# Kernel optimization log

Hardware: AMD Instinct MI355X
Metric: run time of the kernel (lower is better)

## Reference

```python
import jax, jax.numpy as jnp
import numpy as np

Q_DIM, T_DIM, TOP_M, TEMP = 512, 768, 5, 0.07
B, H, W, K = 8, 64, 64, 128
LN_EPS = 1e-5

def _layernorm(x, g, b):
    mu = jnp.mean(x, axis=-1, keepdims=True)
    var = jnp.mean(jnp.square(x - mu), axis=-1, keepdims=True)
    return (x - mu) * jax.lax.rsqrt(var + LN_EPS) * g + b

def _l2norm(x):
    n = jnp.linalg.norm(x, axis=-1, keepdims=True)
    return x / jnp.maximum(n, 1e-12)

def setup_inputs() -> dict:
    key = jax.random.key(0)
    ks = jax.random.split(key, 12)
    s = lambda d: 1.0 / np.sqrt(d)
    return {
        'visual_features': jax.random.normal(ks[0], (B, H, W, Q_DIM), jnp.float32),
        'text_features': jax.random.normal(ks[1], (B, K, T_DIM), jnp.float32),
        'Wq': jax.random.uniform(ks[2], (Q_DIM, T_DIM), jnp.float32, -s(Q_DIM), s(Q_DIM)),
        'bq': jnp.zeros((T_DIM,), jnp.float32),
        'Wv': jax.random.uniform(ks[3], (T_DIM, Q_DIM), jnp.float32, -s(T_DIM), s(T_DIM)),
        'bv': jnp.zeros((Q_DIM,), jnp.float32),
        'W1': jax.random.uniform(ks[4], (Q_DIM, 4 * Q_DIM), jnp.float32, -s(Q_DIM), s(Q_DIM)),
        'b1': jnp.zeros((4 * Q_DIM,), jnp.float32),
        'W2': jax.random.uniform(ks[5], (4 * Q_DIM, Q_DIM), jnp.float32, -s(4 * Q_DIM), s(4 * Q_DIM)),
        'b2': jnp.zeros((Q_DIM,), jnp.float32),
        'g1': jnp.ones((Q_DIM,), jnp.float32), 'be1': jnp.zeros((Q_DIM,), jnp.float32),
        'g2': jnp.ones((Q_DIM,), jnp.float32), 'be2': jnp.zeros((Q_DIM,), jnp.float32),
    }

def reference(visual_features, text_features, Wq, bq, Wv, bv, W1, b1, W2, b2, g1, be1, g2, be2):
    b, h, w, c = visual_features.shape
    residual = visual_features.reshape(b, h * w, c)
    vis = _layernorm(residual, g1, be1)                      # (B,N,C)
    query = _l2norm(vis @ Wq + bq)                            # (B,N,Ct)
    keyt = _l2norm(text_features)                             # (B,K,Ct)
    value = text_features @ Wv + bv                           # (B,K,C)
    sim = jnp.einsum('bnc,bkc->bnk', query, keyt)             # (B,N,K)
    # top-M sparsification: keep top_m logits, others -> -inf
    top_v = jax.lax.top_k(sim, TOP_M)[0]                      # (B,N,M) sorted desc
    thr = top_v[..., -1:]
    sim = jnp.where(sim >= thr, sim, -jnp.inf)
    attn = jax.nn.softmax(sim / TEMP, axis=-1)
    aligned = jnp.einsum('bnk,bkc->bnc', attn, value)
    fused = residual + aligned
    fused = _layernorm(fused, g2, be2)
    ffn = jax.nn.gelu(fused @ W1 + b1, approximate=False) @ W2 + b2
    out = fused + ffn
    return out.reshape(b, h, w, c)
```

## Files before the change

### kernel.cpp

```cpp
#include <hip/hip_runtime.h>
#include <math.h>

typedef unsigned short u16;
typedef unsigned int   u32;
typedef unsigned long long u64;
typedef __attribute__((ext_vector_type(4))) float f32x4;
typedef __attribute__((ext_vector_type(4))) unsigned int u32x4;
typedef __attribute__((ext_vector_type(8))) _Float16 f16x8;
typedef __attribute__((ext_vector_type(8))) short s16x8;

#define NROWS   32768
#define CDIM    512
#define TDIM    768
#define KKEY    128
#define FFDIM   2048
#define NB      8
#define RPB     4096
#define LN_EPS_ 1e-5f
#define TINV    (1.0f/0.07f)
#define RESCUE_MARGIN 1e-5f

__device__ __forceinline__ u16 f2h(float f){ _Float16 h=(_Float16)f; return __builtin_bit_cast(u16,h); }
__device__ __forceinline__ float h2f(u16 v){ return (float)__builtin_bit_cast(_Float16, v); }
__device__ __forceinline__ unsigned pk2(float a,float b){ return (unsigned)f2h(a)|((unsigned)f2h(b)<<16); }
__device__ __forceinline__ u16 f2b(float f){
  u32 u = __builtin_bit_cast(u32, f);
  u32 r = (u + 0x7fffu + ((u>>16)&1u)) >> 16;
  return (u16)r;
}
__device__ __forceinline__ float b2f(u16 h){ u32 u = ((u32)h)<<16; return __builtin_bit_cast(float, u); }
__device__ __forceinline__ unsigned pkb(float a,float b){ return (unsigned)f2b(a)|((unsigned)f2b(b)<<16); }

__device__ __forceinline__ void gl_lds16(const void* g, void* l){
  __builtin_amdgcn_global_load_lds(
      (const __attribute__((address_space(1))) u32*)g,
      (__attribute__((address_space(3))) u32*)l, 16, 0, 0);
}

__device__ __forceinline__ float fast_exp2(float x){
#if __has_builtin(__builtin_amdgcn_exp2f)
  return __builtin_amdgcn_exp2f(x);
#else
  return exp2f(x);
#endif
}
__device__ __forceinline__ float fast_rcp(float x){
#if __has_builtin(__builtin_amdgcn_rcpf)
  return __builtin_amdgcn_rcpf(x);
#else
  return 1.0f/x;
#endif
}

__device__ __forceinline__ float wsumf(float v){
#pragma unroll
  for(int o=1;o<64;o<<=1) v+=__shfl_xor(v,o);
  return v; }
__device__ __forceinline__ float wmaxf(float v){
#pragma unroll
  for(int o=1;o<64;o<<=1) v=fmaxf(v,__shfl_xor(v,o));
  return v; }
__device__ __forceinline__ double wsumd(double v){
#pragma unroll
  for(int o=1;o<64;o<<=1) v+=__shfl_xor(v,o);
  return v; }
__device__ __forceinline__ double wmaxd(double v){
#pragma unroll
  for(int o=1;o<64;o<<=1){ double t=__shfl_xor(v,o); v = t>v ? t : v; }
  return v; }

__device__ __forceinline__ double blocksumd4(double v, double* red){
  const int lane = threadIdx.x & 63, w = threadIdx.x >> 6;
  v = wsumd(v);
  __syncthreads();
  if (lane==0) red[w] = v;
  __syncthreads();
  return red[0]+red[1]+red[2]+red[3];
}

template<int R, int C, int MODE>
__device__ __forceinline__ void tr_tile(const float* __restrict__ in, void* __restrict__ out,
                                        int bx, int by, float (*tile)[33])
{
  int c0 = bx*32, r0 = by*32;
  int tx = threadIdx.x, ty = threadIdx.y;
#pragma unroll
  for (int i=0;i<4;i++){
    int r = r0 + ty + i*8;
    tile[ty+i*8][tx] = in[(size_t)r*C + c0 + tx];
  }
  __syncthreads();
#pragma unroll
  for (int i=0;i<4;i++){
    int cc = c0 + ty + i*8, rr = r0 + tx;
    float v = tile[tx][ty+i*8];
    if (MODE==1)      ((u16*)out)[(size_t)cc*R + rr] = f2h(v);
    else if (MODE==2) ((u16*)out)[(size_t)cc*R + rr] = f2b(v);
    else              ((float*)out)[(size_t)cc*R + rr] = v;
  }
}

__global__ __launch_bounds__(256) void transpose_all_kernel(
    const float* __restrict__ Wq, const float* __restrict__ W1,
    const float* __restrict__ W2, const float* __restrict__ Wv,
    u16* __restrict__ Wqbt, u16* __restrict__ W116t,
    u16* __restrict__ W216t, float* __restrict__ WvT)
{
  __shared__ float tile[32][33];
  int bid = blockIdx.x;
  if (bid < 384){
    tr_tile<512,768,2>(Wq, Wqbt, bid%24, bid/24, tile);
  } else if (bid < 1408){
    int b = bid-384;  tr_tile<512,2048,1>(W1, W116t, b%64, b/64, tile);
  } else if (bid < 2432){
    int b = bid-1408; tr_tile<2048,512,1>(W2, W216t, b%16, b/16, tile);
  } else {
    int b = bid-2432; tr_tile<768,512,0>(Wv, WvT, b%16, b/16, tile);
  }
}

__global__ __launch_bounds__(256) void keystats_kernel(
    const float* __restrict__ text, const float* __restrict__ bq,
    float* __restrict__ normk, float* __restrict__ crr)
{
  int gw = blockIdx.x*4 + (threadIdx.x>>6);
  int lane = threadIdx.x & 63;
  const float* tr = &text[(size_t)gw*TDIM];
  double ss=0.0, db=0.0;
#pragma unroll
  for (int i=0;i<12;i++){
    float v = tr[lane + 64*i];
    ss += (double)v*(double)v;
    db += (double)bq[lane+64*i]*(double)v;
  }
  ss = wsumd(ss); db = wsumd(db);
  if (lane==0){
    double nk = sqrt(ss); nk = nk>1e-12 ? nk : 1e-12;
    normk[gw] = (float)nk;
    crr[gw]   = (float)db;
  }
}

__global__ __launch_bounds__(256) void ln1_kernel(
    const float* __restrict__ visual, const float* __restrict__ g1, const float* __restrict__ be1,
    u16* __restrict__ visH, u16* __restrict__ visL)
{
  int row = blockIdx.x*4 + (threadIdx.x>>6);
  int lane = threadIdx.x & 63;
  size_t base = (size_t)row*CDIM + lane*8;
  f32x4 a = *(const f32x4*)&visual[base];
  f32x4 c = *(const f32x4*)&visual[base+4];
  float s = a[0]+a[1]+a[2]+a[3]+c[0]+c[1]+c[2]+c[3];
  s = wsumf(s);
  float mu = s * (1.0f/512.0f);
  float q = 0.f;
#pragma unroll
  for (int i=0;i<4;i++){ float d=a[i]-mu; q+=d*d; }
#pragma unroll
  for (int i=0;i<4;i++){ float d=c[i]-mu; q+=d*d; }
  q = wsumf(q);
  float rs = rsqrtf(q*(1.0f/512.0f) + LN_EPS_);
  int cb = lane*8;
  float o[8];
#pragma unroll
  for (int i=0;i<4;i++) o[i]   = (a[i]-mu)*rs*g1[cb+i]   + be1[cb+i];
#pragma unroll
  for (int i=0;i<4;i++) o[4+i] = (c[i]-mu)*rs*g1[cb+4+i] + be1[cb+4+i];
  u16 hh[8];
  float lo[8];
#pragma unroll
  for (int i=0;i<8;i++){ hh[i] = f2b(o[i]); lo[i] = o[i] - b2f(hh[i]); }
  u32x4 hv, lv;
#pragma unroll
  for (int i=0;i<4;i++){
    hv[i] = (u32)hh[2*i] | ((u32)hh[2*i+1]<<16);
    lv[i] = pkb(lo[2*i], lo[2*i+1]);
  }
  *(u32x4*)&visH[base] = hv;
  *(u32x4*)&visL[base] = lv;
}

__global__ __launch_bounds__(256) void gemm_txt_kernel(
    const float* __restrict__ text, const float* __restrict__ Wq,
    const float* __restrict__ WvT,
    u16* __restrict__ MrtH, u16* __restrict__ MrtL, float* __restrict__ value)
{
  __shared__ float As[64][17];
  __shared__ float Bs[64][17];
  const int zz = blockIdx.z;
  const bool isV = zz >= 8;
  const int z = isV ? zz-8 : zz;
  const float* A  = text + (size_t)z*KKEY*TDIM;
  const float* Bt = isV ? WvT : Wq;
  const int tid = threadIdx.x;
  const int tx = tid & 15, ty = tid >> 4;
  const int m0 = blockIdx.x*64, n0 = blockIdx.y*64;
  float acc[4][4];
#pragma unroll
  for (int i=0;i<4;i++)
#pragma unroll
    for (int j=0;j<4;j++) acc[i][j]=0.f;
  const int lr = tid >> 2, lc = (tid & 3)*4;
  for (int k0=0; k0<TDIM; k0+=16){
    f32x4 av = *(const f32x4*)&A [(size_t)(m0+lr)*TDIM + k0 + lc];
    f32x4 bv = *(const f32x4*)&Bt[(size_t)(n0+lr)*TDIM + k0 + lc];
#pragma unroll
    for (int i=0;i<4;i++){ As[lr][lc+i]=av[i]; Bs[lr][lc+i]=bv[i]; }
    __syncthreads();
#pragma unroll
    for (int kk=0; kk<16; kk++){
      float a[4], b[4];
#pragma unroll
      for (int i=0;i<4;i++){ a[i]=As[ty*4+i][kk]; b[i]=Bs[tx*4+i][kk]; }
#pragma unroll
      for (int i=0;i<4;i++)
#pragma unroll
        for (int j=0;j<4;j++) acc[i][j] = fmaf(a[i], b[j], acc[i][j]);
    }
    __syncthreads();
  }
#pragma unroll
  for (int i=0;i<4;i++){
    size_t idx = ((size_t)z*KKEY + m0 + ty*4 + i)*CDIM + n0 + tx*4;
    if (isV){
      f32x4 o;
#pragma unroll
      for (int j=0;j<4;j++) o[j]=acc[i][j];
      *(f32x4*)&value[idx] = o;
    } else {
      u16 hh[4]; u16 ll[4];
#pragma unroll
      for (int j=0;j<4;j++){
        float v = acc[i][j];
        u16 h = f2b(v);
        hh[j] = h;
        ll[j] = f2b(v - b2f(h));
      }
      ((u32*)&MrtH[idx])[0] = (u32)hh[0] | ((u32)hh[1]<<16);
      ((u32*)&MrtH[idx])[1] = (u32)hh[2] | ((u32)hh[3]<<16);
      ((u32*)&MrtL[idx])[0] = (u32)ll[0] | ((u32)ll[1]<<16);
      ((u32*)&MrtL[idx])[1] = (u32)ll[2] | ((u32)ll[3]<<16);
    }
  }
}

__device__ __forceinline__ float gelu_exact(float v){
  float x  = v*0.70710678118654752440f;
  float ax = fabsf(x);
  float t  = fast_rcp(fmaf(0.3275911f, ax, 1.0f));
  float p  = t*fmaf(t, fmaf(t, fmaf(t, fmaf(t, 1.061405429f, -1.453152027f),
                  1.421413741f), -0.284496736f), 0.254829592f);
  float e  = fast_exp2(ax*ax*(-1.4426950408889634f));
  float y  = 1.0f - p*e;
  float er = (x < 0.0f) ? -y : y;
  return 0.5f*v*(1.0f + er);
}

template<int EPI, int NN, int KK, int NT>
__global__ __launch_bounds__(256) void gemm_f16_kernel(
    const u16* __restrict__ A, const u16* __restrict__ Bt,
    const float* __restrict__ bias,
    float* __restrict__ out_f,
    u16* __restrict__ out_h,
    const u16* __restrict__ add_h)
{
  __shared__ __align__(16) u16 As[2][128*64];
  __shared__ __align__(16) u16 Bs[2][128*64];
  const int tid = threadIdx.x;
  const int lane = tid & 63, w = tid >> 6;
  const int wr = w >> 1, wc = w & 1;
  constexpr int NWG = 256*NT;
  const int wg = blockIdx.x;
  const int b2 = (wg & 7)*(NWG/8) + (wg >> 3);
  const int ntile = b2 % NT, mtile = b2 / NT;
  const int m0 = mtile*128, n0 = ntile*128;
  f32x4 acc[4][4];
#pragma unroll
  for (int i=0;i<4;i++)
#pragma unroll
    for (int j=0;j<4;j++) acc[i][j] = (f32x4)0.f;
  const int lr = lane & 15, lk = (lane >> 4)*8;
  const int c8_sw = ((lane & 7) ^ (lane >> 3))*8;
  const size_t stride32 = (size_t)32*KK;
  const u16* aBase = &A [(size_t)(m0 + w*8 + (lane>>3))*KK + c8_sw];
  const u16* bBase = &Bt[(size_t)(n0 + w*8 + (lane>>3))*KK + c8_sw];

  auto STAGE = [&](int buf, int k0){
#pragma unroll
    for (int i=0;i<4;i++){
      gl_lds16(aBase + i*stride32 + k0, &As[buf][w*512 + i*2048]);
      gl_lds16(bBase + i*stride32 + k0, &Bs[buf][w*512 + i*2048]);
    }
  };

  STAGE(0, 0);
  int cur = 0;
  for (int k0=0; k0<KK; k0+=64){
    if (k0 + 64 < KK){
      STAGE(cur^1, k0+64);
      asm volatile("s_waitcnt vmcnt(8)" ::: "memory");
    } else {
      asm volatile("s_waitcnt vmcnt(0)" ::: "memory");
    }
    __builtin_amdgcn_s_barrier();
#pragma unroll
    for (int kk=0; kk<64; kk+=32){
      s16x8 af[4], bfv[4];
      const int csw = (kk + lk) ^ ((lr & 7) << 3);
#pragma unroll
      for (int mi=0;mi<4;mi++) af[mi]  = *(const s16x8*)&As[cur][(wr*64 + mi*16 + lr)*64 + csw];
#pragma unroll
      for (int ni=0;ni<4;ni++) bfv[ni] = *(const s16x8*)&Bs[cur][(wc*64 + ni*16 + lr)*64 + csw];
#pragma unroll
      for (int mi=0;mi<4;mi++)
#pragma unroll
        for (int ni=0;ni<4;ni++){
          if (EPI == 0)
            acc[mi][ni] = __builtin_amdgcn_mfma_f32_16x16x32_bf16(af[mi], bfv[ni], acc[mi][ni], 0, 0, 0);
          else
            acc[mi][ni] = __builtin_amdgcn_mfma_f32_16x16x32_f16(
                __builtin_bit_cast(f16x8, af[mi]), __builtin_bit_cast(f16x8, bfv[ni]), acc[mi][ni], 0, 0, 0);
        }
    }
    __builtin_amdgcn_s_barrier();
    cur ^= 1;
  }
  const int lr4 = (lane >> 4)*4;
  if (EPI == 0){
    float sq[4][4];
#pragma unroll
    for (int mi=0;mi<4;mi++)
#pragma unroll
      for (int r=0;r<4;r++) sq[mi][r]=0.f;
#pragma unroll
    for (int ni=0;ni<4;ni++){
      float bqv = bias[n0 + wc*64 + ni*16 + lr];
#pragma unroll
      for (int mi=0;mi<4;mi++)
#pragma unroll
        for (int r=0;r<4;r++){
          float v = acc[mi][ni][r] + bqv;
          sq[mi][r] += v*v;
        }
    }
#pragma unroll
    for (int o=1;o<16;o<<=1)
#pragma unroll
      for (int mi=0;mi<4;mi++)
#pragma unroll
        for (int r=0;r<4;r++) sq[mi][r] += __shfl_xor(sq[mi][r], o);
    if ((lane & 15) == 0){
      int part = ntile*2 + wc;
#pragma unroll
      for (int mi=0;mi<4;mi++)
#pragma unroll
        for (int r=0;r<4;r++){
          int row = m0 + wr*64 + mi*16 + lr4 + r;
          out_f[(size_t)row*12 + part] = sq[mi][r];
        }
    }
  } else {
    const int row0 = m0 + wr*64 + lr4;
    const int col0 = n0 + wc*64 + lr;
    float bb[4];
#pragma unroll
    for (int ni=0;ni<4;ni++) bb[ni] = bias[col0 + ni*16];
    if (EPI == 1){
      u16* op = out_h + (size_t)row0*NN + col0;
#pragma unroll
      for (int mi=0;mi<4;mi++)
#pragma unroll
        for (int r=0;r<4;r++)
#pragma unroll
          for (int ni=0;ni<4;ni++)
            op[(size_t)(mi*16+r)*NN + ni*16] = f2h(gelu_exact(acc[mi][ni][r] + bb[ni]));
    } else {
      float* op = out_f + (size_t)row0*NN + col0;
      const u16* rp = add_h + (size_t)row0*NN + col0;
#pragma unroll
      for (int mi=0;mi<4;mi++)
#pragma unroll
        for (int r=0;r<4;r++)
#pragma unroll
          for (int ni=0;ni<4;ni++)
            op[(size_t)(mi*16+r)*NN + ni*16] =
                acc[mi][ni][r] + bb[ni] + h2f(rp[(size_t)(mi*16+r)*NN + ni*16]);
    }
  }
}

__global__ __launch_bounds__(256) void gemm_t_kernel(
    const u16* __restrict__ Ah, const u16* __restrict__ Al,
    const u16* __restrict__ Bh, const u16* __restrict__ Bl,
    float* __restrict__ C)
{
  __shared__ __align__(16) u16 As[2][128*64];
  __shared__ __align__(16) u16 Bs[2][128*64];
  const int tid = threadIdx.x;
  const int lane = tid & 63, w = tid >> 6;
  const int wr = w >> 1, wc = w & 1;
  const int mtile = blockIdx.x;
  const int p = blockIdx.y;
  const int m0 = mtile*128, z = mtile >> 5;
  const u16* Ap = (p==2) ? Al : Ah;
  const u16* Bp = (p==1) ? Bl : Bh;
  f32x4 acc[4][4];
#pragma unroll
  for (int i=0;i<4;i++)
#pragma unroll
    for (int j=0;j<4;j++) acc[i][j] = (f32x4)0.f;
  const int lr = lane & 15, lk = (lane >> 4)*8;
  const int c8_sw = ((lane & 7) ^ (lane >> 3))*8;
  const size_t aOff = (size_t)(m0 + w*8 + (lane>>3))*CDIM + c8_sw;
  const size_t bOff = (size_t)(z*KKEY + w*8 + (lane>>3))*CDIM + c8_sw;
  const size_t stride32 = (size_t)32*CDIM;

  auto STAGE = [&](int buf, int s){
    const int k0 = s << 6;
#pragma unroll
    for (int i=0;i<4;i++){
      gl_lds16(Ap + aOff + i*stride32 + k0, &As[buf][w*512 + i*2048]);
      gl_lds16(Bp + bOff + i*stride32 + k0, &Bs[buf][w*512 + i*2048]);
    }
  };

  STAGE(0, 0);
  int cur = 0;
  for (int s=0; s<8; ++s){
    if (s < 7){
      STAGE(cur^1, s+1);
      asm volatile("s_waitcnt vmcnt(8)" ::: "memory");
    } else {
      asm volatile("s_waitcnt vmcnt(0)" ::: "memory");
    }
    __builtin_amdgcn_s_barrier();
#pragma unroll
    for (int kk=0; kk<64; kk+=32){
      s16x8 af[4], bfv[4];
      const int csw = (kk + lk) ^ ((lr & 7) << 3);
#pragma unroll
      for (int mi=0;mi<4;mi++) af[mi]  = *(const s16x8*)&As[cur][(wr*64 + mi*16 + lr)*64 + csw];
#pragma unroll
      for (int ni=0;ni<4;ni++) bfv[ni] = *(const s16x8*)&Bs[cur][(wc*64 + ni*16 + lr)*64 + csw];
#pragma unroll
      for (int mi=0;mi<4;mi++)
#pragma unroll
        for (int ni=0;ni<4;ni++)
          acc[mi][ni] = __builtin_amdgcn_mfma_f32_16x16x32_bf16(af[mi], bfv[ni], acc[mi][ni], 0, 0, 0);
    }
    __builtin_amdgcn_s_barrier();
    cur ^= 1;
  }
  const int lr4 = (lane >> 4)*4;
  const int row0 = m0 + wr*64 + lr4;
  const int col0 = wc*64 + lr;
  float* op = C + (size_t)p*NROWS*KKEY + (size_t)row0*KKEY + col0;
#pragma unroll
  for (int mi=0;mi<4;mi++)
#pragma unroll
    for (int r=0;r<4;r++)
#pragma unroll
      for (int ni=0;ni<4;ni++)
        op[(size_t)(mi*16+r)*KKEY + ni*16] = acc[mi][ni][r];
}

__global__ __launch_bounds__(256) void rescue_kernel(
    const int* __restrict__ rcnt, const int* __restrict__ rlist,
    const float* __restrict__ visual, const float* __restrict__ text,
    const float* __restrict__ Wq, const float* __restrict__ bq,
    const float* __restrict__ g1, const float* __restrict__ be1,
    const float* __restrict__ g2, const float* __restrict__ be2,
    const float* __restrict__ value, const float* __restrict__ bv,
    u16* __restrict__ fused16)
{
  __shared__ double vis64[512];
  __shared__ double q64[768];
  __shared__ double sims[128];
  __shared__ double pw[128];
  __shared__ double red[4];
  __shared__ double sc2[2];
  __shared__ int klist[128];
  __shared__ int kcount;
  const int tid = threadIdx.x, lane = tid & 63, w = tid >> 6;
  int n = *rcnt; if (n > NROWS) n = NROWS;
  for (int i = blockIdx.x; i < n; i += gridDim.x){
    const int row = rlist[i], b = row >> 12;
    const size_t rb = (size_t)row*CDIM;
    double x0 = (double)visual[rb+tid], x1 = (double)visual[rb+tid+256];
    double s = blocksumd4(x0+x1, red);
    double mu = s*(1.0/512.0);
    double d0 = x0-mu, d1 = x1-mu;
    double var = blocksumd4(d0*d0+d1*d1, red);
    double rs = 1.0/sqrt(var*(1.0/512.0) + 1e-5);
    vis64[tid]     = d0*rs*(double)g1[tid]     + (double)be1[tid];
    vis64[tid+256] = d1*rs*(double)g1[tid+256] + (double)be1[tid+256];
    __syncthreads();
    double qa0=(double)bq[tid], qa1=(double)bq[tid+256], qa2=(double)bq[tid+512];
#pragma unroll 4
    for (int c=0;c<CDIM;c++){
      double v = vis64[c];
      const float* wrow = &Wq[(size_t)c*TDIM];
      qa0 += v*(double)wrow[tid];
      qa1 += v*(double)wrow[tid+256];
      qa2 += v*(double)wrow[tid+512];
    }
    q64[tid]=qa0; q64[tid+256]=qa1; q64[tid+512]=qa2;
    double nq2 = blocksumd4(qa0*qa0+qa1*qa1+qa2*qa2, red);
    double nq = sqrt(nq2); if (nq < 1e-12) nq = 1e-12;
    __syncthreads();
    if (tid < KKEY){
      const float* trow = &text[((size_t)b*KKEY + tid)*TDIM];
      double dot=0.0, nk2=0.0;
#pragma unroll 8
      for (int j=0;j<TDIM;j++){
        double tv = (double)trow[j];
        dot += q64[j]*tv; nk2 += tv*tv;
      }
      double nk = sqrt(nk2); if (nk < 1e-12) nk = 1e-12;
      sims[tid] = dot/(nq*nk);
    }
    __syncthreads();
    if (w == 0){
      double v0=sims[lane], v1=sims[lane+64];
      bool rm0=false, rm1=false;
      double thr=0.0, smax=0.0;
      for (int it=0; it<5; ++it){
        double c0 = rm0 ? -1e300 : v0;
        double c1 = rm1 ? -1e300 : v1;
        double m = wmaxd(c0>c1 ? c0 : c1);
        if (it==0) smax = m;
        thr = m;
        bool h0 = (!rm0) && (v0==m);
        u64 k0 = __ballot(h0);
        if (k0){ if (lane == __ffsll(k0)-1) rm0 = true; }
        else {
          bool h1 = (!rm1) && (v1==m);
          u64 k1 = __ballot(h1);
          if (lane == __ffsll(k1)-1) rm1 = true;
        }
      }
      if (lane==0){ sc2[0]=smax; sc2[1]=thr; kcount=0; }
    }
    __syncthreads();
    const double smax = sc2[0], thr = sc2[1];
    double p = 0.0;
    if (tid < KKEY){
      double sv = sims[tid];
      p = (sv >= thr) ? exp((sv-smax)*(1.0/0.07)) : 0.0;
      pw[tid] = p;
      if (p > 0.0){ int pos = atomicAdd(&kcount, 1); klist[pos] = tid; }
    }
    double Z = blocksumd4(p, red);
    double zi = 1.0/Z;
    __syncthreads();
    double a0=(double)bv[tid], a1=(double)bv[tid+256];
    int kc = kcount;
    for (int ki=0; ki<kc; ++ki){
      int k = klist[ki];
      double wt = pw[k]*zi;
      const float* vr = &value[((size_t)b*KKEY + k)*CDIM];
      a0 += wt*(double)vr[tid];
      a1 += wt*(double)vr[tid+256];
    }
    double f0 = (double)visual[rb+tid]     + a0;
    double f1 = (double)visual[rb+tid+256] + a1;
    double fsum = blocksumd4(f0+f1, red);
    double fmu = fsum*(1.0/512.0);
    double e0=f0-fmu, e1=f1-fmu;
    double fvar = blocksumd4(e0*e0+e1*e1, red);
    double frs = 1.0/sqrt(fvar*(1.0/512.0) + 1e-5);
    fused16[rb+tid]     = f2h((float)(e0*frs*(double)g2[tid]     + (double)be2[tid]));
    fused16[rb+tid+256] = f2h((float)(e1*frs*(double)g2[tid+256] + (double)be2[tid+256]));
    __syncthreads();
  }
}

__global__ __launch_bounds__(256) void attn_ln2_kernel(
    const float* __restrict__ visual,
    const float* __restrict__ tbuf, const float* __restrict__ crr,
    const float* __restrict__ normk, const float* __restrict__ qpart,
    const float* __restrict__ value, const float* __restrict__ bv,
    const float* __restrict__ g2, const float* __restrict__ be2,
    u16* __restrict__ fused16,
    int* __restrict__ rcnt, int* __restrict__ rlist)
{
  const int w = threadIdx.x >> 6, lane = threadIdx.x & 63;
  const int row = blockIdx.x*4 + w;
  const int b = row >> 12;
  float nqp = (lane < 12) ? qpart[(size_t)row*12 + lane] : 0.f;
  float nq2 = wsumf(nqp);
  float nq = fmaxf(sqrtf(nq2), 1e-12f);
  const float* t0 = &tbuf[(size_t)row*KKEY];
  const float* t1 = t0 + (size_t)NROWS*KKEY;
  const float* t2 = t1 + (size_t)NROWS*KKEY;
  float ta = t0[lane]    + t1[lane]    + t2[lane];
  float tb = t0[lane+64] + t1[lane+64] + t2[lane+64];
  float s0 = (ta + crr[b*KKEY + lane])    / (nq*normk[b*KKEY + lane]);
  float s1 = (tb + crr[b*KKEY + lane+64]) / (nq*normk[b*KKEY + lane+64]);
  float v0=s0, v1=s1; bool rm0=false, rm1=false;
  float thr=0.f, smax=0.f, m6=0.f;
  for (int it=0; it<6; ++it){
    float c0 = rm0 ? -1e30f : v0;
    float c1 = rm1 ? -1e30f : v1;
    float m = wmaxf(fmaxf(c0,c1));
    if (it==0) smax = m;
    if (it<5){
      thr = m;
      bool h0 = (!rm0) && (v0==m);
      u64 k0 = __ballot(h0);
      if (k0){ if (lane == __ffsll(k0)-1) rm0 = true; }
      else {
        bool h1 = (!rm1) && (v1==m);
        u64 k1 = __ballot(h1);
        if (lane == __ffsll(k1)-1) rm1 = true;
      }
    } else m6 = m;
  }
  if ((thr - m6) < RESCUE_MARGIN){
    if (lane == 0){
      int p = atomicAdd(rcnt, 1);
      rlist[p] = row;
    }
    return;
  }
  float p0 = (s0>=thr) ? expf((s0-smax)*TINV) : 0.f;
  float p1 = (s1>=thr) ? expf((s1-smax)*TINV) : 0.f;
  float Z = wsumf(p0+p1);
  float zi = 1.f/Z;
  float accv[8];
#pragma unroll
  for (int j=0;j<8;j++) accv[j] = bv[lane*8+j];
  u64 mk0 = __ballot(p0>0.f);
  u64 mk1 = __ballot(p1>0.f);
  while (mk0){
    int l = __ffsll(mk0)-1; mk0 &= mk0-1;
    float wt = __shfl(p0, l)*zi;
    const f32x4* vr = (const f32x4*)&value[((size_t)b*KKEY + l)*CDIM + lane*8];
    f32x4 va = vr[0], vb = vr[1];
#pragma unroll
    for (int j=0;j<4;j++){ accv[j] += wt*va[j]; accv[4+j] += wt*vb[j]; }
  }
  while (mk1){
    int l = __ffsll(mk1)-1; mk1 &= mk1-1;
    float wt = __shfl(p1, l)*zi;
    const f32x4* vr = (const f32x4*)&value[((size_t)b*KKEY + l + 64)*CDIM + lane*8];
    f32x4 va = vr[0], vb = vr[1];
#pragma unroll
    for (int j=0;j<4;j++){ accv[j] += wt*va[j]; accv[4+j] += wt*vb[j]; }
  }
  size_t rb = (size_t)row*CDIM + lane*8;
  f32x4 r0v = *(const f32x4*)&visual[rb];
  f32x4 r1v = *(const f32x4*)&visual[rb+4];
  float f[8];
#pragma unroll
  for (int j=0;j<4;j++){ f[j]=r0v[j]+accv[j]; f[4+j]=r1v[j]+accv[4+j]; }
  float fs=0.f;
#pragma unroll
  for (int j=0;j<8;j++) fs += f[j];
  fs = wsumf(fs);
  float fmu = fs*(1.0f/512.0f);
  float fvv=0.f;
#pragma unroll
  for (int j=0;j<8;j++){ float d=f[j]-fmu; fvv+=d*d; }
  fvv = wsumf(fvv);
  float frs = rsqrtf(fvv*(1.0f/512.0f) + LN_EPS_);
  int cb = lane*8;
  f32x4 o0,o1;
#pragma unroll
  for (int j=0;j<4;j++) o0[j] = (f[j]-fmu)*frs*g2[cb+j]     + be2[cb+j];
#pragma unroll
  for (int j=0;j<4;j++) o1[j] = (f[4+j]-fmu)*frs*g2[cb+4+j] + be2[cb+4+j];
  u32x4 hv;
  hv[0]=pk2(o0[0],o0[1]); hv[1]=pk2(o0[2],o0[3]);
  hv[2]=pk2(o1[0],o1[1]); hv[3]=pk2(o1[2],o1[3]);
  *(u32x4*)&fused16[rb] = hv;
}

extern "C" void kernel_launch(void* const* d_in, const int* in_sizes, int n_in,
                              void* d_out, int out_size, void* d_ws, size_t ws_size,
                              hipStream_t stream)
{
  (void)in_sizes; (void)n_in; (void)out_size; (void)ws_size;
  const float* visual = (const float*)d_in[0];
  const float* text   = (const float*)d_in[1];
  const float* Wq     = (const float*)d_in[2];
  const float* bq     = (const float*)d_in[3];
  const float* Wv     = (const float*)d_in[4];
  const float* bv     = (const float*)d_in[5];
  const float* W1     = (const float*)d_in[6];
  const float* b1     = (const float*)d_in[7];
  const float* W2     = (const float*)d_in[8];
  const float* b2     = (const float*)d_in[9];
  const float* g1     = (const float*)d_in[10];
  const float* be1    = (const float*)d_in[11];
  const float* g2     = (const float*)d_in[12];
  const float* be2    = (const float*)d_in[13];
  float* out = (float*)d_out;

  char* ws = (char*)d_ws;
  size_t off = 0;
  auto alloc = [&](size_t bytes)->char*{
    char* p = ws + off; off += (bytes + 255) & ~(size_t)255; return p; };

  u16*    visH   = (u16*)   alloc((size_t)NROWS*CDIM*2);
  u16*    visL   = (u16*)   alloc((size_t)NROWS*CDIM*2);
  u16*    h16    = (u16*)   alloc((size_t)NROWS*FFDIM*2);
  u16*    fused16= (u16*)   alloc((size_t)NROWS*CDIM*2);
  u16*    MrtH   = (u16*)   alloc((size_t)NB*KKEY*CDIM*2);
  u16*    MrtL   = (u16*)   alloc((size_t)NB*KKEY*CDIM*2);
  float*  value  = (float*) alloc((size_t)NB*KKEY*CDIM*4);
  u16*    Wqbt   = (u16*)   alloc((size_t)TDIM*CDIM*2);
  u16*    W116t  = (u16*)   alloc((size_t)FFDIM*CDIM*2);
  u16*    W216t  = (u16*)   alloc((size_t)CDIM*FFDIM*2);
  float*  WvT    = (float*) alloc((size_t)CDIM*TDIM*4);
  float*  qpart  = (float*) alloc((size_t)NROWS*12*4);
  float*  normk  = (float*) alloc((size_t)NB*KKEY*4);
  float*  crr    = (float*) alloc((size_t)NB*KKEY*4);
  int*    rcnt   = (int*)   alloc(256);
  int*    rlist  = (int*)   alloc((size_t)NROWS*4);
  float*  tbuf   = (float*)h16;

  hipMemsetAsync(rcnt, 0, sizeof(int), stream);

  transpose_all_kernel<<<2816, dim3(32,8), 0, stream>>>(
      Wq, W1, W2, Wv, Wqbt, W116t, W216t, WvT);
  keystats_kernel<<<256, 256, 0, stream>>>(text, bq, normk, crr);
  gemm_txt_kernel<<<dim3(2, 8, 16), 256, 0, stream>>>(
      text, Wq, WvT, MrtH, MrtL, value);
  ln1_kernel<<<NROWS/4, 256, 0, stream>>>(visual, g1, be1, visH, visL);
  gemm_t_kernel<<<dim3(256, 3), 256, 0, stream>>>(visH, visL, MrtH, MrtL, tbuf);
  gemm_f16_kernel<0,TDIM,CDIM,6><<<1536, 256, 0, stream>>>(
      visH, Wqbt, bq, qpart, nullptr, nullptr);
  attn_ln2_kernel<<<NROWS/4, 256, 0, stream>>>(
      visual, tbuf, crr, normk, qpart, value, bv, g2, be2,
      fused16, rcnt, rlist);
  rescue_kernel<<<256, 256, 0, stream>>>(
      rcnt, rlist, visual, text, Wq, bq, g1, be1, g2, be2, value, bv, fused16);
  gemm_f16_kernel<1,FFDIM,CDIM,16><<<4096, 256, 0, stream>>>(
      fused16, W116t, b1, nullptr, h16, nullptr);
  gemm_f16_kernel<2,CDIM,FFDIM,4><<<1024, 256, 0, stream>>>(
      h16, W216t, b2, out, nullptr, fused16);
}
```

Before: 458.6 us.

## Make GEMM blocks loop over several N tiles and fold split-precision passes

Each GEMM workgroup now processes several consecutive 128-column output tiles (TPB per block), with one continuous double-buffered pipeline across tiles and an epilogue after each tile. Grids shrink to 512 blocks, which cuts launch and prologue overhead and keeps the A tile warm in cache. The split-precision similarity GEMM now accumulates its three hi/lo passes in registers inside one block instead of writing three partial buffers. That removes the 3x tbuf traffic and the summation in the attention kernel. The trade-off is less parallelism per GEMM and epilogue stalls in the middle of the pipeline.

```diff
diff --git a/kernel.cpp b/kernel.cpp
--- a/kernel.cpp
+++ b/kernel.cpp
@@ -256,7 +256,7 @@
   return 0.5f*v*(1.0f + er);
 }
 
-template<int EPI, int NN, int KK, int NT>
+template<int EPI, int NN, int KK, int NT, int TPB>
 __global__ __launch_bounds__(256) void gemm_f16_kernel(
     const u16* __restrict__ A, const u16* __restrict__ Bt,
     const float* __restrict__ bias,
@@ -266,14 +266,17 @@
 {
   __shared__ __align__(16) u16 As[2][128*64];
   __shared__ __align__(16) u16 Bs[2][128*64];
+  constexpr int KSTEPS = KK/64;
+  constexpr int BPM = NT/TPB;
+  constexpr int NWG = 256*BPM;
+  constexpr int GTOT = TPB*KSTEPS;
   const int tid = threadIdx.x;
   const int lane = tid & 63, w = tid >> 6;
   const int wr = w >> 1, wc = w & 1;
-  constexpr int NWG = 256*NT;
   const int wg = blockIdx.x;
   const int b2 = (wg & 7)*(NWG/8) + (wg >> 3);
-  const int ntile = b2 % NT, mtile = b2 / NT;
-  const int m0 = mtile*128, n0 = ntile*128;
+  const int mtile = b2 / BPM, nb = (b2 % BPM)*TPB;
+  const int m0 = mtile*128;
   f32x4 acc[4][4];
 #pragma unroll
   for (int i=0;i<4;i++)
@@ -282,22 +285,27 @@
   const int lr = lane & 15, lk = (lane >> 4)*8;
   const int c8_sw = ((lane & 7) ^ (lane >> 3))*8;
   const size_t stride32 = (size_t)32*KK;
-  const u16* aBase = &A [(size_t)(m0 + w*8 + (lane>>3))*KK + c8_sw];
-  const u16* bBase = &Bt[(size_t)(n0 + w*8 + (lane>>3))*KK + c8_sw];
-
-  auto STAGE = [&](int buf, int k0){
+  const int rowoff = w*8 + (lane>>3);
+  const u16* aBase = &A [(size_t)(m0 + rowoff)*KK + c8_sw];
+  const u16* bBase = &Bt[(size_t)(nb*128 + rowoff)*KK + c8_sw];
+
+  auto STAGE = [&](int g, int buf){
+    const int t = g / KSTEPS, k0 = (g & (KSTEPS-1))*64;
+    const u16* ap = aBase + k0;
+    const u16* bp = bBase + (size_t)t*128*KK + k0;
 #pragma unroll
     for (int i=0;i<4;i++){
-      gl_lds16(aBase + i*stride32 + k0, &As[buf][w*512 + i*2048]);
-      gl_lds16(bBase + i*stride32 + k0, &Bs[buf][w*512 + i*2048]);
+      gl_lds16(ap + i*stride32, &As[buf][w*512 + i*2048]);
+      gl_lds16(bp + i*stride32, &Bs[buf][w*512 + i*2048]);
     }
   };
 
+  const int lr4 = (lane >> 4)*4;
   STAGE(0, 0);
-  int cur = 0;
-  for (int k0=0; k0<KK; k0+=64){
-    if (k0 + 64 < KK){
-      STAGE(cur^1, k0+64);
+  for (int g=0; g<GTOT; ++g){
+    const int cur = g & 1;
+    if (g+1 < GTOT){
+      STAGE(g+1, cur^1);
       asm volatile("s_waitcnt vmcnt(8)" ::: "memory");
     } else {
       asm volatile("s_waitcnt vmcnt(0)" ::: "memory");
@@ -323,68 +331,74 @@
         }
     }
     __builtin_amdgcn_s_barrier();
-    cur ^= 1;
-  }
-  const int lr4 = (lane >> 4)*4;
-  if (EPI == 0){
-    float sq[4][4];
-#pragma unroll
-    for (int mi=0;mi<4;mi++)
-#pragma unroll
-      for (int r=0;r<4;r++) sq[mi][r]=0.f;
-#pragma unroll
-    for (int ni=0;ni<4;ni++){
-      float bqv = bias[n0 + wc*64 + ni*16 + lr];
-#pragma unroll
-      for (int mi=0;mi<4;mi++)
-#pragma unroll
-        for (int r=0;r<4;r++){
-          float v = acc[mi][ni][r] + bqv;
-          sq[mi][r] += v*v;
+    if ((g & (KSTEPS-1)) == KSTEPS-1){
+      const int ntile = nb + g/KSTEPS;
+      const int n0 = ntile*128;
+      if (EPI == 0){
+        float sq[4][4];
+#pragma unroll
+        for (int mi=0;mi<4;mi++)
+#pragma unroll
+          for (int r=0;r<4;r++) sq[mi][r]=0.f;
+#pragma unroll
+        for (int ni=0;ni<4;ni++){
+          float bqv = bias[n0 + wc*64 + ni*16 + lr];
+#pragma unroll
+          for (int mi=0;mi<4;mi++)
+#pragma unroll
+            for (int r=0;r<4;r++){
+              float v = acc[mi][ni][r] + bqv;
+              sq[mi][r] += v*v;
+            }
         }
-    }
-#pragma unroll
-    for (int o=1;o<16;o<<=1)
-#pragma unroll
-      for (int mi=0;mi<4;mi++)
-#pragma unroll
-        for (int r=0;r<4;r++) sq[mi][r] += __shfl_xor(sq[mi][r], o);
-    if ((lane & 15) == 0){
-      int part = ntile*2 + wc;
-#pragma unroll
-      for (int mi=0;mi<4;mi++)
-#pragma unroll
-        for (int r=0;r<4;r++){
-          int row = m0 + wr*64 + mi*16 + lr4 + r;
-          out_f[(size_t)row*12 + part] = sq[mi][r];
+#pragma unroll
+        for (int o=1;o<16;o<<=1)
+#pragma unroll
+          for (int mi=0;mi<4;mi++)
+#pragma unroll
+            for (int r=0;r<4;r++) sq[mi][r] += __shfl_xor(sq[mi][r], o);
+        if ((lane & 15) == 0){
+          int part = ntile*2 + wc;
+#pragma unroll
+          for (int mi=0;mi<4;mi++)
+#pragma unroll
+            for (int r=0;r<4;r++){
+              int row = m0 + wr*64 + mi*16 + lr4 + r;
+              out_f[(size_t)row*12 + part] = sq[mi][r];
+            }
         }
-    }
-  } else {
-    const int row0 = m0 + wr*64 + lr4;
-    const int col0 = n0 + wc*64 + lr;
-    float bb[4];
-#pragma unroll
-    for (int ni=0;ni<4;ni++) bb[ni] = bias[col0 + ni*16];
-    if (EPI == 1){
-      u16* op = out_h + (size_t)row0*NN + col0;
-#pragma unroll
-      for (int mi=0;mi<4;mi++)
-#pragma unroll
-        for (int r=0;r<4;r++)
-#pragma unroll
-          for (int ni=0;ni<4;ni++)
-            op[(size_t)(mi*16+r)*NN + ni*16] = f2h(gelu_exact(acc[mi][ni][r] + bb[ni]));
-    } else {
-      float* op = out_f + (size_t)row0*NN + col0;
-      const u16* rp = add_h + (size_t)row0*NN + col0;
-#pragma unroll
-      for (int mi=0;mi<4;mi++)
-#pragma unroll
-        for (int r=0;r<4;r++)
-#pragma unroll
-          for (int ni=0;ni<4;ni++)
-            op[(size_t)(mi*16+r)*NN + ni*16] =
-                acc[mi][ni][r] + bb[ni] + h2f(rp[(size_t)(mi*16+r)*NN + ni*16]);
+      } else {
+        const int row0 = m0 + wr*64 + lr4;
+        const int col0 = n0 + wc*64 + lr;
+        float bb[4];
+#pragma unroll
+        for (int ni=0;ni<4;ni++) bb[ni] = bias[col0 + ni*16];
+        if (EPI == 1){
+          u16* op = out_h + (size_t)row0*NN + col0;
+#pragma unroll
+          for (int mi=0;mi<4;mi++)
+#pragma unroll
+            for (int r=0;r<4;r++)
+#pragma unroll
+              for (int ni=0;ni<4;ni++)
+                op[(size_t)(mi*16+r)*NN + ni*16] = f2h(gelu_exact(acc[mi][ni][r] + bb[ni]));
+        } else {
+          float* op = out_f + (size_t)row0*NN + col0;
+          const u16* rp = add_h + (size_t)row0*NN + col0;
+#pragma unroll
+          for (int mi=0;mi<4;mi++)
+#pragma unroll
+            for (int r=0;r<4;r++)
+#pragma unroll
+              for (int ni=0;ni<4;ni++)
+                op[(size_t)(mi*16+r)*NN + ni*16] =
+                    acc[mi][ni][r] + bb[ni] + h2f(rp[(size_t)(mi*16+r)*NN + ni*16]);
+        }
+      }
+#pragma unroll
+      for (int i=0;i<4;i++)
+#pragma unroll
+        for (int j=0;j<4;j++) acc[i][j] = (f32x4)0.f;
     }
   }
 }
@@ -399,11 +413,9 @@
   const int tid = threadIdx.x;
   const int lane = tid & 63, w = tid >> 6;
   const int wr = w >> 1, wc = w & 1;
-  const int mtile = blockIdx.x;
-  const int p = blockIdx.y;
+  const int wg = blockIdx.x;
+  const int mtile = (wg & 7)*32 + (wg >> 3);
   const int m0 = mtile*128, z = mtile >> 5;
-  const u16* Ap = (p==2) ? Al : Ah;
-  const u16* Bp = (p==1) ? Bl : Bh;
   f32x4 acc[4][4];
 #pragma unroll
   for (int i=0;i<4;i++)
@@ -411,12 +423,15 @@
     for (int j=0;j<4;j++) acc[i][j] = (f32x4)0.f;
   const int lr = lane & 15, lk = (lane >> 4)*8;
   const int c8_sw = ((lane & 7) ^ (lane >> 3))*8;
-  const size_t aOff = (size_t)(m0 + w*8 + (lane>>3))*CDIM + c8_sw;
-  const size_t bOff = (size_t)(z*KKEY + w*8 + (lane>>3))*CDIM + c8_sw;
+  const int rowoff = w*8 + (lane>>3);
+  const size_t aOff = (size_t)(m0 + rowoff)*CDIM + c8_sw;
+  const size_t bOff = (size_t)(z*KKEY + rowoff)*CDIM + c8_sw;
   const size_t stride32 = (size_t)32*CDIM;
 
-  auto STAGE = [&](int buf, int s){
-    const int k0 = s << 6;
+  auto STAGE = [&](int g, int buf){
+    const int p = g >> 3, k0 = (g & 7) << 6;
+    const u16* Ap = (p==2) ? Al : Ah;
+    const u16* Bp = (p==1) ? Bl : Bh;
 #pragma unroll
     for (int i=0;i<4;i++){
       gl_lds16(Ap + aOff + i*stride32 + k0, &As[buf][w*512 + i*2048]);
@@ -425,10 +440,10 @@
   };
 
   STAGE(0, 0);
-  int cur = 0;
-  for (int s=0; s<8; ++s){
-    if (s < 7){
-      STAGE(cur^1, s+1);
+  for (int g=0; g<24; ++g){
+    const int cur = g & 1;
+    if (g < 23){
+      STAGE(g+1, cur^1);
       asm volatile("s_waitcnt vmcnt(8)" ::: "memory");
     } else {
       asm volatile("s_waitcnt vmcnt(0)" ::: "memory");
@@ -449,12 +464,11 @@
           acc[mi][ni] = __builtin_amdgcn_mfma_f32_16x16x32_bf16(af[mi], bfv[ni], acc[mi][ni], 0, 0, 0);
     }
     __builtin_amdgcn_s_barrier();
-    cur ^= 1;
   }
   const int lr4 = (lane >> 4)*4;
   const int row0 = m0 + wr*64 + lr4;
   const int col0 = wc*64 + lr;
-  float* op = C + (size_t)p*NROWS*KKEY + (size_t)row0*KKEY + col0;
+  float* op = C + (size_t)row0*KKEY + col0;
 #pragma unroll
   for (int mi=0;mi<4;mi++)
 #pragma unroll
@@ -590,13 +604,9 @@
   float nqp = (lane < 12) ? qpart[(size_t)row*12 + lane] : 0.f;
   float nq2 = wsumf(nqp);
   float nq = fmaxf(sqrtf(nq2), 1e-12f);
-  const float* t0 = &tbuf[(size_t)row*KKEY];
-  const float* t1 = t0 + (size_t)NROWS*KKEY;
-  const float* t2 = t1 + (size_t)NROWS*KKEY;
-  float ta = t0[lane]    + t1[lane]    + t2[lane];
-  float tb = t0[lane+64] + t1[lane+64] + t2[lane+64];
-  float s0 = (ta + crr[b*KKEY + lane])    / (nq*normk[b*KKEY + lane]);
-  float s1 = (tb + crr[b*KKEY + lane+64]) / (nq*normk[b*KKEY + lane+64]);
+  const float* trow = &tbuf[(size_t)row*KKEY];
+  float s0 = (trow[lane]    + crr[b*KKEY + lane])    / (nq*normk[b*KKEY + lane]);
+  float s1 = (trow[lane+64] + crr[b*KKEY + lane+64]) / (nq*normk[b*KKEY + lane+64]);
   float v0=s0, v1=s1; bool rm0=false, rm1=false;
   float thr=0.f, smax=0.f, m6=0.f;
   for (int it=0; it<6; ++it){
@@ -728,16 +738,16 @@
   gemm_txt_kernel<<<dim3(2, 8, 16), 256, 0, stream>>>(
       text, Wq, WvT, MrtH, MrtL, value);
   ln1_kernel<<<NROWS/4, 256, 0, stream>>>(visual, g1, be1, visH, visL);
-  gemm_t_kernel<<<dim3(256, 3), 256, 0, stream>>>(visH, visL, MrtH, MrtL, tbuf);
-  gemm_f16_kernel<0,TDIM,CDIM,6><<<1536, 256, 0, stream>>>(
+  gemm_t_kernel<<<256, 256, 0, stream>>>(visH, visL, MrtH, MrtL, tbuf);
+  gemm_f16_kernel<0,TDIM,CDIM,6,3><<<512, 256, 0, stream>>>(
       visH, Wqbt, bq, qpart, nullptr, nullptr);
   attn_ln2_kernel<<<NROWS/4, 256, 0, stream>>>(
       visual, tbuf, crr, normk, qpart, value, bv, g2, be2,
       fused16, rcnt, rlist);
   rescue_kernel<<<256, 256, 0, stream>>>(
       rcnt, rlist, visual, text, Wq, bq, g1, be1, g2, be2, value, bv, fused16);
-  gemm_f16_kernel<1,FFDIM,CDIM,16><<<4096, 256, 0, stream>>>(
+  gemm_f16_kernel<1,FFDIM,CDIM,16,8><<<512, 256, 0, stream>>>(
       fused16, W116t, b1, nullptr, h16, nullptr);
-  gemm_f16_kernel<2,CDIM,FFDIM,4><<<1024, 256, 0, stream>>>(
+  gemm_f16_kernel<2,CDIM,FFDIM,4,2><<<512, 256, 0, stream>>>(
       h16, W216t, b2, out, nullptr, fused16);
 }
```

Result: slower. 504.6 us (+10.0%).

## Accumulate split-precision GEMM passes in one block and drop partial buffers

Applied to the files above, without the earlier changes.

The three hi/lo split-precision product passes of the similarity GEMM now run inside a single workgroup as one 24-step K loop into a single accumulator, instead of three separate grid slices that each write a partial result. The downstream attention kernel then reads one fp32 tile instead of summing three. This removes two full N×K fp32 writes and reads. The block-to-tile mapping is also swizzled so concurrently running blocks touch different batches. The cost is a third as many blocks (256) each doing three times the work, which may underfill the GPU.

```diff
diff --git a/kernel.cpp b/kernel.cpp
--- a/kernel.cpp
+++ b/kernel.cpp
@@ -399,11 +399,9 @@
   const int tid = threadIdx.x;
   const int lane = tid & 63, w = tid >> 6;
   const int wr = w >> 1, wc = w & 1;
-  const int mtile = blockIdx.x;
-  const int p = blockIdx.y;
+  const int wg = blockIdx.x;
+  const int mtile = (wg & 7)*32 + (wg >> 3);
   const int m0 = mtile*128, z = mtile >> 5;
-  const u16* Ap = (p==2) ? Al : Ah;
-  const u16* Bp = (p==1) ? Bl : Bh;
   f32x4 acc[4][4];
 #pragma unroll
   for (int i=0;i<4;i++)
@@ -411,12 +409,15 @@
     for (int j=0;j<4;j++) acc[i][j] = (f32x4)0.f;
   const int lr = lane & 15, lk = (lane >> 4)*8;
   const int c8_sw = ((lane & 7) ^ (lane >> 3))*8;
-  const size_t aOff = (size_t)(m0 + w*8 + (lane>>3))*CDIM + c8_sw;
-  const size_t bOff = (size_t)(z*KKEY + w*8 + (lane>>3))*CDIM + c8_sw;
+  const int rowoff = w*8 + (lane>>3);
+  const size_t aOff = (size_t)(m0 + rowoff)*CDIM + c8_sw;
+  const size_t bOff = (size_t)(z*KKEY + rowoff)*CDIM + c8_sw;
   const size_t stride32 = (size_t)32*CDIM;
 
-  auto STAGE = [&](int buf, int s){
-    const int k0 = s << 6;
+  auto STAGE = [&](int g, int buf){
+    const int p = g >> 3, k0 = (g & 7) << 6;
+    const u16* Ap = (p==2) ? Al : Ah;
+    const u16* Bp = (p==1) ? Bl : Bh;
 #pragma unroll
     for (int i=0;i<4;i++){
       gl_lds16(Ap + aOff + i*stride32 + k0, &As[buf][w*512 + i*2048]);
@@ -425,10 +426,10 @@
   };
 
   STAGE(0, 0);
-  int cur = 0;
-  for (int s=0; s<8; ++s){
-    if (s < 7){
-      STAGE(cur^1, s+1);
+  for (int g=0; g<24; ++g){
+    const int cur = g & 1;
+    if (g < 23){
+      STAGE(g+1, cur^1);
       asm volatile("s_waitcnt vmcnt(8)" ::: "memory");
     } else {
       asm volatile("s_waitcnt vmcnt(0)" ::: "memory");
@@ -449,12 +450,11 @@
           acc[mi][ni] = __builtin_amdgcn_mfma_f32_16x16x32_bf16(af[mi], bfv[ni], acc[mi][ni], 0, 0, 0);
     }
     __builtin_amdgcn_s_barrier();
-    cur ^= 1;
   }
   const int lr4 = (lane >> 4)*4;
   const int row0 = m0 + wr*64 + lr4;
   const int col0 = wc*64 + lr;
-  float* op = C + (size_t)p*NROWS*KKEY + (size_t)row0*KKEY + col0;
+  float* op = C + (size_t)row0*KKEY + col0;
 #pragma unroll
   for (int mi=0;mi<4;mi++)
 #pragma unroll
@@ -590,13 +590,9 @@
   float nqp = (lane < 12) ? qpart[(size_t)row*12 + lane] : 0.f;
   float nq2 = wsumf(nqp);
   float nq = fmaxf(sqrtf(nq2), 1e-12f);
-  const float* t0 = &tbuf[(size_t)row*KKEY];
-  const float* t1 = t0 + (size_t)NROWS*KKEY;
-  const float* t2 = t1 + (size_t)NROWS*KKEY;
-  float ta = t0[lane]    + t1[lane]    + t2[lane];
-  float tb = t0[lane+64] + t1[lane+64] + t2[lane+64];
-  float s0 = (ta + crr[b*KKEY + lane])    / (nq*normk[b*KKEY + lane]);
-  float s1 = (tb + crr[b*KKEY + lane+64]) / (nq*normk[b*KKEY + lane+64]);
+  const float* trow = &tbuf[(size_t)row*KKEY];
+  float s0 = (trow[lane]    + crr[b*KKEY + lane])    / (nq*normk[b*KKEY + lane]);
+  float s1 = (trow[lane+64] + crr[b*KKEY + lane+64]) / (nq*normk[b*KKEY + lane+64]);
   float v0=s0, v1=s1; bool rm0=false, rm1=false;
   float thr=0.f, smax=0.f, m6=0.f;
   for (int it=0; it<6; ++it){
@@ -728,7 +724,7 @@
   gemm_txt_kernel<<<dim3(2, 8, 16), 256, 0, stream>>>(
       text, Wq, WvT, MrtH, MrtL, value);
   ln1_kernel<<<NROWS/4, 256, 0, stream>>>(visual, g1, be1, visH, visL);
-  gemm_t_kernel<<<dim3(256, 3), 256, 0, stream>>>(visH, visL, MrtH, MrtL, tbuf);
+  gemm_t_kernel<<<256, 256, 0, stream>>>(visH, visL, MrtH, MrtL, tbuf);
   gemm_f16_kernel<0,TDIM,CDIM,6><<<1536, 256, 0, stream>>>(
       visH, Wqbt, bq, qpart, nullptr, nullptr);
   attn_ln2_kernel<<<NROWS/4, 256, 0, stream>>>(
```

New measurement: 459.6 us. Within noise of the previous version (+0.2%).
